# Kernel tuning notes

Hardware: AMD Instinct MI355X
Metric: run time of the kernel (lower is better)

Reference implementation:

```python
import jax, jax.numpy as jnp
import numpy as np

N, E, F_IN, H, D = 50000, 800000, 128, 4, 32


def setup_inputs() -> dict:
    key = jax.random.key(0)
    k_x, k_e, k_w, k_al, k_ar = jax.random.split(key, 5)
    x = jax.random.normal(k_x, (N, F_IN), dtype=jnp.float32)
    edge_index = jax.random.randint(k_e, (2, E), 0, N, dtype=jnp.int32).astype(jnp.int64)
    # xavier-uniform-like scales
    s_w = float(np.sqrt(6.0 / (F_IN + H * D)))
    s_a = float(np.sqrt(6.0 / (D + 1)))
    W = jax.random.uniform(k_w, (F_IN, H * D), jnp.float32, -s_w, s_w)
    att_l = jax.random.uniform(k_al, (H, D), jnp.float32, -s_a, s_a)
    att_r = jax.random.uniform(k_ar, (H, D), jnp.float32, -s_a, s_a)
    bias = jnp.zeros((H * D,), jnp.float32)
    return {"x": x, "edge_index": edge_index, "W": W, "att_l": att_l, "att_r": att_r, "bias": bias}


def reference(x, edge_index, W, att_l, att_r, bias):
    num_nodes = x.shape[0]
    n_heads, head_dim = att_l.shape
    h = (x @ W).reshape(num_nodes, n_heads, head_dim)          # [N,H,D]
    alpha_l = jnp.einsum('nhd,hd->nh', h, att_l)               # [N,H]
    alpha_r = jnp.einsum('nhd,hd->nh', h, att_r)               # [N,H]
    from_idx, to_idx = edge_index[0], edge_index[1]
    att = alpha_l[from_idx] + alpha_r[to_idx]                  # [E,H]
    att = jax.nn.leaky_relu(att, negative_slope=0.2)
    # segment softmax over edges grouped by destination node (shift by global
    # per-head max, exactly as the source's _softmax effectively does)
    att = att - jax.lax.stop_gradient(jnp.max(att, axis=0, keepdims=True))
    ex = jnp.exp(att)                                          # [E,H]
    denom = jax.ops.segment_sum(ex, to_idx, num_segments=num_nodes)  # [N,H]
    att_n = ex / (denom[to_idx] + 1e-9)                        # [E,H]
    # scatter-weighted aggregation: out[n] = sum_{e: to=n} att[e] * h[from[e]]
    msgs = att_n[:, :, None] * h[from_idx]                     # [E,H,D]
    out = jax.ops.segment_sum(msgs, to_idx, num_segments=num_nodes)  # [N,H,D]
    out = out.reshape(num_nodes, n_heads * head_dim) + bias
    return out
```

## Files before the change

### kernel.cpp

```cpp
#include <hip/hip_runtime.h>
#include <cstdint>

#define N_NODES 50000
#define N_EDGES 800000
#define F_IN    128
#define N_HEADS 4
#define HEAD_DIM 32
#define F_OUT   128

#define NBUCK   391
#define NPB     128
#define KA_GRID 512
#define EPB     1563
#define CAPA    24
#define REC_CAP 2560
#define STAGE_CAP REC_CAP
#define NSTRIP  (N_NODES / 16)
#define NGEMM   ((NSTRIP + 3) / 4)

typedef unsigned int uint32;
typedef unsigned short ushort;
typedef __attribute__((ext_vector_type(8))) short short8v;
typedef __attribute__((ext_vector_type(4))) float float4v;

typedef __attribute__((address_space(1))) const ushort gushort;
typedef __attribute__((address_space(3))) ushort lushort;

__device__ __forceinline__ ushort f2bf(float f) {
    uint32 u = __float_as_uint(f);
    return (ushort)((u + 0x7FFFu + ((u >> 16) & 1u)) >> 16);
}


__device__ __forceinline__ int block_scan_excl_256(int v, int* p_total)
{
    const int t = threadIdx.x, lane = t & 63, wv = t >> 6;
    int incl = v;
#pragma unroll
    for (int d = 1; d < 64; d <<= 1) {
        int u = __shfl_up(incl, d);
        if (lane >= d) incl += u;
    }
    __shared__ int wsum[4];
    if (lane == 63) wsum[wv] = incl;
    __syncthreads();
    int woff = 0;
#pragma unroll
    for (int j = 0; j < 4; ++j) {
        int s = wsum[j];
        if (j < wv) woff += s;
    }
    if (p_total) *p_total = wsum[0] + wsum[1] + wsum[2] + wsum[3];
    __syncthreads();
    return woff + incl - v;
}

__global__ __launch_bounds__(256) void k_prep(const float* __restrict__ W,
    ushort* __restrict__ WTF)
{
    const int id = blockIdx.x * 256 + threadIdx.x;
    if (id >= 32 * 64) return;
    const int tile = id >> 6, l = id & 63;
    const int q = l >> 4, c15 = l & 15;
    const int nt = tile >> 2, kt = tile & 3;
    short8v hv, lv;
#pragma unroll
    for (int j = 0; j < 8; ++j) {
        const int k = kt * 32 + q * 8 + j;
        const float w = W[k * F_OUT + nt * 16 + c15];
        const ushort hi = f2bf(w);
        const float hif = __uint_as_float((uint32)hi << 16);
        hv[j] = (short)hi;
        lv[j] = (short)f2bf(w - hif);
    }
    *(short8v*)&WTF[tile * 512 + l * 8]         = hv;
    *(short8v*)&WTF[16384 + tile * 512 + l * 8] = lv;
}

__global__ __launch_bounds__(256, 2) void k_bin_gemm(
    const int* __restrict__ ei, const float* __restrict__ x,
    const ushort* __restrict__ WTF,
    const float* __restrict__ attl, const float* __restrict__ attr,
    uint32* __restrict__ priv, int* __restrict__ cnts,
    uint32* __restrict__ hbq, float* __restrict__ aLp, float* __restrict__ aRp)
{
    __shared__ __attribute__((aligned(16))) char lds_buf[65536];

    if (blockIdx.x < KA_GRID) {
        int* cur = (int*)lds_buf;
        const int sb = blockIdx.x, t = threadIdx.x;
        for (int bb = t; bb < NBUCK; bb += 256) cur[bb] = 0;
        __syncthreads();
        const int e0 = sb * EPB;
        const int lim = min(EPB, N_EDGES - e0);
        for (int i = t; i < lim; i += 256) {
            const int from = ei[e0 + i];
            const int to   = ei[N_EDGES + e0 + i];
            const int b = to >> 7;
            const int slot = atomicAdd(&cur[b], 1);
            if (slot < CAPA)
                priv[((size_t)b * KA_GRID + sb) * CAPA + slot] =
                    (uint32)from | ((uint32)(to & 127) << 16);
        }
        __syncthreads();
        for (int bb = t; bb < NBUCK; bb += 256)
            cnts[sb * NBUCK + bb] = min(cur[bb], CAPA);
        return;
    }

    const int bid   = blockIdx.x - KA_GRID;
    const int lane  = threadIdx.x & 63;
    const int wv    = threadIdx.x >> 6;
    const int q     = lane >> 4;
    const int c15   = lane & 15;

    ushort* wt = (ushort*)lds_buf;
#pragma unroll
    for (int i = 0; i < 16; ++i) {
        const int chunk = wv * 16 + i;
        __builtin_amdgcn_global_load_lds(
            (gushort*)(WTF + chunk * 512 + lane * 8),
            (lushort*)(wt + chunk * 512), 16, 0, 0);
    }
    __syncthreads();

    const int strip = bid * 4 + wv;
    if (strip >= NSTRIP) return;
    const int row0 = strip * 16;

    const float* xrow = x + (size_t)(row0 + c15) * F_IN + q * 8;
    short8v ahi[4], alo[4];
#pragma unroll
    for (int kt = 0; kt < 4; ++kt) {
        const float4 f0 = *(const float4*)(xrow + kt * 32);
        const float4 f1 = *(const float4*)(xrow + kt * 32 + 4);
        const float fs[8] = {f0.x, f0.y, f0.z, f0.w, f1.x, f1.y, f1.z, f1.w};
#pragma unroll
        for (int j = 0; j < 8; ++j) {
            const ushort hi = f2bf(fs[j]);
            const float hif = __uint_as_float((uint32)hi << 16);
            ahi[kt][j] = (short)hi;
            alo[kt][j] = (short)f2bf(fs[j] - hif);
        }
    }

    float4v acc[8];
#pragma unroll
    for (int nt = 0; nt < 8; ++nt) {
        float4v a = {0.f, 0.f, 0.f, 0.f};
#pragma unroll
        for (int kt = 0; kt < 4; ++kt) {
            const short8v bh = *(const short8v*)(wt + (nt * 4 + kt) * 512 + lane * 8);
            const short8v bl = *(const short8v*)(wt + 16384 + (nt * 4 + kt) * 512 + lane * 8);
            a = __builtin_amdgcn_mfma_f32_16x16x32_bf16(ahi[kt], bh, a, 0, 0, 0);
            a = __builtin_amdgcn_mfma_f32_16x16x32_bf16(alo[kt], bh, a, 0, 0, 0);
            a = __builtin_amdgcn_mfma_f32_16x16x32_bf16(ahi[kt], bl, a, 0, 0, 0);
        }
        acc[nt] = a;
    }

#pragma unroll
    for (int nt = 0; nt < 4; ++nt) {
#pragma unroll
        for (int r = 0; r < 4; ++r) {
            const uint32 d = (uint32)f2bf(acc[nt][r]) | ((uint32)f2bf(acc[nt + 4][r]) << 16);
            hbq[(size_t)(row0 + q * 4 + r) * 64 + nt * 16 + c15] = d;
        }
    }

    float aLacc[4][4] = {{0.f}}, aRacc[4][4] = {{0.f}};
#pragma unroll
    for (int nt = 0; nt < 8; ++nt) {
        const float alv = attl[nt * 16 + c15];
        const float arv = attr[nt * 16 + c15];
        const int hh = nt >> 1;
#pragma unroll
        for (int r = 0; r < 4; ++r) {
            aLacc[r][hh] = fmaf(acc[nt][r], alv, aLacc[r][hh]);
            aRacc[r][hh] = fmaf(acc[nt][r], arv, aRacc[r][hh]);
        }
    }
#pragma unroll
    for (int r = 0; r < 4; ++r) {
#pragma unroll
        for (int hh = 0; hh < 4; ++hh) {
            float vl = aLacc[r][hh], vr = aRacc[r][hh];
#pragma unroll
            for (int d = 1; d < 16; d <<= 1) {
                vl += __shfl_xor(vl, d);
                vr += __shfl_xor(vr, d);
            }
            if (c15 == hh) {
                const int row = row0 + q * 4 + r;
                const int pos = (hh & 1) * 2 + (hh >> 1);
                aLp[row * N_HEADS + pos] = vl;
                aRp[row * N_HEADS + pos] = vr;
            }
        }
    }
}

__global__ __launch_bounds__(256) void k_build(const uint32* __restrict__ priv,
    const int* __restrict__ cnts,
    int* __restrict__ count, int* __restrict__ offsets, int* __restrict__ rec_from)
{
    __shared__ uint32 stage[STAGE_CAP];
    __shared__ int so_s[KA_GRID];
    __shared__ ushort cts_s[KA_GRID];
    __shared__ int hist[NPB], curn[NPB];
    const int b = blockIdx.x, t = threadIdx.x;

    int c[2], s = 0;
#pragma unroll
    for (int j = 0; j < 2; ++j) {
        c[j] = cnts[(size_t)(2 * t + j) * NBUCK + b];
        s += c[j];
    }
    int total;
    int ex = block_scan_excl_256(s, &total);
#pragma unroll
    for (int j = 0; j < 2; ++j) {
        so_s[2 * t + j]  = ex;
        cts_s[2 * t + j] = (ushort)c[j];
        ex += c[j];
    }
    if (t < NPB) hist[t] = 0;
    __syncthreads();

    const uint32* pbase = priv + (size_t)b * KA_GRID * CAPA;
    for (int idx = t; idx < KA_GRID * CAPA; idx += 256) {
        const int sb = idx / CAPA;
        const int sl = idx - sb * CAPA;
        if (sl < (int)cts_s[sb]) {
            const int p = so_s[sb] + sl;
            if (p < STAGE_CAP) stage[p] = pbase[idx];
        }
    }
    __syncthreads();

    const int S = min(total, STAGE_CAP);
    for (int i = t; i < S; i += 256) atomicAdd(&hist[stage[i] >> 16], 1);
    __syncthreads();

    const int hv = (t < NPB) ? hist[t] : 0;
    int tot2;
    const int lo = block_scan_excl_256(hv, &tot2);
    const int rbase = b * REC_CAP;
    const int n = b * NPB + t;
    if (t < NPB && n < N_NODES) {
        count[n]   = hv;
        offsets[n] = rbase + lo;
    }
    if (t < NPB) curn[t] = lo;
    __syncthreads();

    for (int i = t; i < S; i += 256) {
        const uint32 e = stage[i];
        const int pos = atomicAdd(&curn[e >> 16], 1);
        rec_from[rbase + pos] = (int)(e & 0xFFFFu);
    }
}

__global__ __launch_bounds__(256) void k_agg(const int* __restrict__ rec_from,
    const int* __restrict__ count, const int* __restrict__ offsets,
    const float* __restrict__ aLp, const float* __restrict__ aRp,
    const uint32* __restrict__ hbq,
    const float* __restrict__ bias, float* __restrict__ out)
{
    const int lane = threadIdx.x & 63;
    const int n = blockIdx.x * 4 + (threadIdx.x >> 6);
    if (n >= N_NODES) return;
    const int cnt  = count[n];
    const int off  = offsets[n];
    const int hsel = (lane >> 5) * 2;
    const int l31  = lane & 31;
    const int gsel = lane & 32;
    const float2 arv = *(const float2*)&aRp[n * N_HEADS + hsel];
    float ax = 0.f, ay = 0.f, ds0 = 0.f, ds1 = 0.f;

    for (int base = 0; base < cnt; base += 32) {
        const int m = min(32, cnt - base);
        int vf = 0;
        float e0p = 0.f, e1p = 0.f;
        if (l31 < m) {
            vf = rec_from[off + base + l31];
            const float2 af = *(const float2*)&aLp[vf * N_HEADS + hsel];
            float t0 = af.x + arv.x; t0 = (t0 > 0.f) ? t0 : 0.2f * t0;
            float t1 = af.y + arv.y; t1 = (t1 > 0.f) ? t1 : 0.2f * t1;
            e0p = __expf(t0);
            e1p = __expf(t1);
        }
        int i = 0;
        for (; i + 8 <= m; i += 8) {
            int f[8]; uint32 h[8]; float e0[8], e1[8];
#pragma unroll
            for (int j = 0; j < 8; ++j) {
                const int s = gsel | (i + j);
                f[j]  = __shfl(vf, s);
                e0[j] = __shfl(e0p, s);
                e1[j] = __shfl(e1p, s);
            }
#pragma unroll
            for (int j = 0; j < 8; ++j) h[j] = hbq[(size_t)f[j] * 64 + lane];
#pragma unroll
            for (int j = 0; j < 8; ++j) {
                ax = fmaf(e0[j], __uint_as_float(h[j] << 16), ax);
                ay = fmaf(e1[j], __uint_as_float(h[j] & 0xFFFF0000u), ay);
                ds0 += e0[j]; ds1 += e1[j];
            }
        }
        for (; i + 4 <= m; i += 4) {
            int f[4]; uint32 h[4]; float e0[4], e1[4];
#pragma unroll
            for (int j = 0; j < 4; ++j) {
                const int s = gsel | (i + j);
                f[j]  = __shfl(vf, s);
                e0[j] = __shfl(e0p, s);
                e1[j] = __shfl(e1p, s);
            }
#pragma unroll
            for (int j = 0; j < 4; ++j) h[j] = hbq[(size_t)f[j] * 64 + lane];
#pragma unroll
            for (int j = 0; j < 4; ++j) {
                ax = fmaf(e0[j], __uint_as_float(h[j] << 16), ax);
                ay = fmaf(e1[j], __uint_as_float(h[j] & 0xFFFF0000u), ay);
                ds0 += e0[j]; ds1 += e1[j];
            }
        }
        for (; i < m; ++i) {
            const int s = gsel | i;
            const int f = __shfl(vf, s);
            const uint32 hv = hbq[(size_t)f * 64 + lane];
            const float e0 = __shfl(e0p, s), e1 = __shfl(e1p, s);
            ax = fmaf(e0, __uint_as_float(hv << 16), ax);
            ay = fmaf(e1, __uint_as_float(hv & 0xFFFF0000u), ay);
            ds0 += e0; ds1 += e1;
        }
    }
    const float inv0 = 1.0f / (ds0 + 1e-9f);
    const float inv1 = 1.0f / (ds1 + 1e-9f);
    out[n * F_OUT + lane]      = ax * inv0 + bias[lane];
    out[n * F_OUT + 64 + lane] = ay * inv1 + bias[64 + lane];
}

extern "C" void kernel_launch(void* const* d_in, const int* in_sizes, int n_in,
                              void* d_out, int out_size, void* d_ws, size_t ws_size,
                              hipStream_t stream)
{
    const float* x    = (const float*)d_in[0];
    const int*   ei   = (const int*)d_in[1];
    const float* W    = (const float*)d_in[2];
    const float* attl = (const float*)d_in[3];
    const float* attr = (const float*)d_in[4];
    const float* bias = (const float*)d_in[5];
    float* out = (float*)d_out;

    char* p = (char*)d_ws;
    auto carve = [&](size_t bytes) -> char* {
        char* q = p;
        p += (bytes + 255) & ~size_t(255);
        return q;
    };
    uint32* hbq      = (uint32*)carve((size_t)N_NODES * 64 * 4);
    uint32* priv     = (uint32*)carve((size_t)NBUCK * KA_GRID * CAPA * 4);
    int*    rec_from = (int*)carve((size_t)NBUCK * REC_CAP * 4);
    ushort* WTF      = (ushort*)carve(32768 * 2);
    float*  aLp      = (float*)carve((size_t)N_NODES * N_HEADS * 4);
    float*  aRp      = (float*)carve((size_t)N_NODES * N_HEADS * 4);
    int*    cnts     = (int*)carve((size_t)KA_GRID * NBUCK * 4);
    int*    count    = (int*)carve((size_t)N_NODES * 4);
    int*    offsets  = (int*)carve((size_t)N_NODES * 4);

    k_prep<<<8, 256, 0, stream>>>(W, WTF);
    k_bin_gemm<<<KA_GRID + NGEMM, 256, 0, stream>>>(ei, x, WTF,
                                                    attl, attr, priv, cnts,
                                                    hbq, aLp, aRp);
    k_build<<<NBUCK, 256, 0, stream>>>(priv, cnts, count, offsets, rec_from);
    k_agg<<<(N_NODES + 3) / 4, 256, 0, stream>>>(rec_from, count, offsets,
                                                 aLp, aRp, hbq, bias, out);
}
```

Before: 163.9 us.

## Widen bin/GEMM blocks to 512 threads, reorder roles, use LDS broadcast in aggregation

```diff
diff --git a/kernel.cpp b/kernel.cpp
--- a/kernel.cpp
+++ b/kernel.cpp
@@ -16,7 +16,7 @@
 #define REC_CAP 2560
 #define STAGE_CAP REC_CAP
 #define NSTRIP  (N_NODES / 16)
-#define NGEMM   ((NSTRIP + 3) / 4)
+#define NGEMM   ((NSTRIP + 7) / 8)
 
 typedef unsigned int uint32;
 typedef unsigned short ushort;
@@ -77,7 +77,7 @@
     *(short8v*)&WTF[16384 + tile * 512 + l * 8] = lv;
 }
 
-__global__ __launch_bounds__(256, 2) void k_bin_gemm(
+__global__ __launch_bounds__(512, 4) void k_bin_gemm(
     const int* __restrict__ ei, const float* __restrict__ x,
     const ushort* __restrict__ WTF,
     const float* __restrict__ attl, const float* __restrict__ attr,
@@ -86,14 +86,14 @@
 {
     __shared__ __attribute__((aligned(16))) char lds_buf[65536];
 
-    if (blockIdx.x < KA_GRID) {
+    if (blockIdx.x >= NGEMM) {
         int* cur = (int*)lds_buf;
-        const int sb = blockIdx.x, t = threadIdx.x;
-        for (int bb = t; bb < NBUCK; bb += 256) cur[bb] = 0;
+        const int sb = blockIdx.x - NGEMM, t = threadIdx.x;
+        for (int bb = t; bb < NBUCK; bb += 512) cur[bb] = 0;
         __syncthreads();
         const int e0 = sb * EPB;
         const int lim = min(EPB, N_EDGES - e0);
-        for (int i = t; i < lim; i += 256) {
+        for (int i = t; i < lim; i += 512) {
             const int from = ei[e0 + i];
             const int to   = ei[N_EDGES + e0 + i];
             const int b = to >> 7;
@@ -103,12 +103,12 @@
                     (uint32)from | ((uint32)(to & 127) << 16);
         }
         __syncthreads();
-        for (int bb = t; bb < NBUCK; bb += 256)
+        for (int bb = t; bb < NBUCK; bb += 512)
             cnts[sb * NBUCK + bb] = min(cur[bb], CAPA);
         return;
     }
 
-    const int bid   = blockIdx.x - KA_GRID;
+    const int bid   = blockIdx.x;
     const int lane  = threadIdx.x & 63;
     const int wv    = threadIdx.x >> 6;
     const int q     = lane >> 4;
@@ -116,15 +116,15 @@
 
     ushort* wt = (ushort*)lds_buf;
 #pragma unroll
-    for (int i = 0; i < 16; ++i) {
-        const int chunk = wv * 16 + i;
+    for (int i = 0; i < 8; ++i) {
+        const int chunk = wv * 8 + i;
         __builtin_amdgcn_global_load_lds(
             (gushort*)(WTF + chunk * 512 + lane * 8),
             (lushort*)(wt + chunk * 512), 16, 0, 0);
     }
     __syncthreads();
 
-    const int strip = bid * 4 + wv;
+    const int strip = bid * 8 + wv;
     if (strip >= NSTRIP) return;
     const int row0 = strip * 16;
 
@@ -267,74 +267,65 @@
     const uint32* __restrict__ hbq,
     const float* __restrict__ bias, float* __restrict__ out)
 {
+    __shared__ float4 ebuf[4][2][32];
     const int lane = threadIdx.x & 63;
-    const int n = blockIdx.x * 4 + (threadIdx.x >> 6);
+    const int wvb  = threadIdx.x >> 6;
+    const int n = blockIdx.x * 4 + wvb;
     if (n >= N_NODES) return;
     const int cnt  = count[n];
     const int off  = offsets[n];
-    const int hsel = (lane >> 5) * 2;
+    const int hb   = lane >> 5;
+    const int hsel = hb * 2;
     const int l31  = lane & 31;
-    const int gsel = lane & 32;
     const float2 arv = *(const float2*)&aRp[n * N_HEADS + hsel];
     float ax = 0.f, ay = 0.f, ds0 = 0.f, ds1 = 0.f;
 
     for (int base = 0; base < cnt; base += 32) {
         const int m = min(32, cnt - base);
-        int vf = 0;
-        float e0p = 0.f, e1p = 0.f;
         if (l31 < m) {
-            vf = rec_from[off + base + l31];
+            const int vf = rec_from[off + base + l31];
             const float2 af = *(const float2*)&aLp[vf * N_HEADS + hsel];
             float t0 = af.x + arv.x; t0 = (t0 > 0.f) ? t0 : 0.2f * t0;
             float t1 = af.y + arv.y; t1 = (t1 > 0.f) ? t1 : 0.2f * t1;
-            e0p = __expf(t0);
-            e1p = __expf(t1);
-        }
+            ebuf[wvb][hb][l31] = make_float4(__int_as_float(vf),
+                                             __expf(t0), __expf(t1), 0.f);
+        }
+        __asm volatile("s_waitcnt lgkmcnt(0)" ::: "memory");
         int i = 0;
         for (; i + 8 <= m; i += 8) {
-            int f[8]; uint32 h[8]; float e0[8], e1[8];
+            float4 r[8]; uint32 h[8];
+#pragma unroll
+            for (int j = 0; j < 8; ++j) r[j] = ebuf[wvb][hb][i + j];
+#pragma unroll
+            for (int j = 0; j < 8; ++j)
+                h[j] = hbq[(size_t)__float_as_int(r[j].x) * 64 + lane];
 #pragma unroll
             for (int j = 0; j < 8; ++j) {
-                const int s = gsel | (i + j);
-                f[j]  = __shfl(vf, s);
-                e0[j] = __shfl(e0p, s);
-                e1[j] = __shfl(e1p, s);
+                ax = fmaf(r[j].y, __uint_as_float(h[j] << 16), ax);
+                ay = fmaf(r[j].z, __uint_as_float(h[j] & 0xFFFF0000u), ay);
+                ds0 += r[j].y; ds1 += r[j].z;
             }
-#pragma unroll
-            for (int j = 0; j < 8; ++j) h[j] = hbq[(size_t)f[j] * 64 + lane];
-#pragma unroll
-            for (int j = 0; j < 8; ++j) {
-                ax = fmaf(e0[j], __uint_as_float(h[j] << 16), ax);
-                ay = fmaf(e1[j], __uint_as_float(h[j] & 0xFFFF0000u), ay);
-                ds0 += e0[j]; ds1 += e1[j];
+        }
+        for (; i + 4 <= m; i += 4) {
+            float4 r[4]; uint32 h[4];
+#pragma unroll
+            for (int j = 0; j < 4; ++j) r[j] = ebuf[wvb][hb][i + j];
+#pragma unroll
+            for (int j = 0; j < 4; ++j)
+                h[j] = hbq[(size_t)__float_as_int(r[j].x) * 64 + lane];
+#pragma unroll
+            for (int j = 0; j < 4; ++j) {
+                ax = fmaf(r[j].y, __uint_as_float(h[j] << 16), ax);
+                ay = fmaf(r[j].z, __uint_as_float(h[j] & 0xFFFF0000u), ay);
+                ds0 += r[j].y; ds1 += r[j].z;
             }
         }
-        for (; i + 4 <= m; i += 4) {
-            int f[4]; uint32 h[4]; float e0[4], e1[4];
-#pragma unroll
-            for (int j = 0; j < 4; ++j) {
-                const int s = gsel | (i + j);
-                f[j]  = __shfl(vf, s);
-                e0[j] = __shfl(e0p, s);
-                e1[j] = __shfl(e1p, s);
-            }
-#pragma unroll
-            for (int j = 0; j < 4; ++j) h[j] = hbq[(size_t)f[j] * 64 + lane];
-#pragma unroll
-            for (int j = 0; j < 4; ++j) {
-                ax = fmaf(e0[j], __uint_as_float(h[j] << 16), ax);
-                ay = fmaf(e1[j], __uint_as_float(h[j] & 0xFFFF0000u), ay);
-                ds0 += e0[j]; ds1 += e1[j];
-            }
-        }
         for (; i < m; ++i) {
-            const int s = gsel | i;
-            const int f = __shfl(vf, s);
-            const uint32 hv = hbq[(size_t)f * 64 + lane];
-            const float e0 = __shfl(e0p, s), e1 = __shfl(e1p, s);
-            ax = fmaf(e0, __uint_as_float(hv << 16), ax);
-            ay = fmaf(e1, __uint_as_float(hv & 0xFFFF0000u), ay);
-            ds0 += e0; ds1 += e1;
+            const float4 r = ebuf[wvb][hb][i];
+            const uint32 hv = hbq[(size_t)__float_as_int(r.x) * 64 + lane];
+            ax = fmaf(r.y, __uint_as_float(hv << 16), ax);
+            ay = fmaf(r.z, __uint_as_float(hv & 0xFFFF0000u), ay);
+            ds0 += r.y; ds1 += r.z;
         }
     }
     const float inv0 = 1.0f / (ds0 + 1e-9f);
@@ -372,7 +363,7 @@
     int*    offsets  = (int*)carve((size_t)N_NODES * 4);
 
     k_prep<<<8, 256, 0, stream>>>(W, WTF);
-    k_bin_gemm<<<KA_GRID + NGEMM, 256, 0, stream>>>(ei, x, WTF,
+    k_bin_gemm<<<NGEMM + KA_GRID, 512, 0, stream>>>(ei, x, WTF,
                                                     attl, attr, priv, cnts,
                                                     hbq, aLp, aRp);
     k_build<<<NBUCK, 256, 0, stream>>>(priv, cnts, count, offsets, rec_from);
```

Measured after the change: 167.2 us. 1.02x slower.
